# Kernel tuning notes

Hardware: AMD Instinct MI355X
Metric: run time of the kernel (lower is better)

The kernel has to match this reference:

```python
import jax, jax.numpy as jnp
import numpy as np

N, E = 50000, 800000
IN_CH, H, OUT_CH, ED, L = 64, 128, 128, 1, 4


def setup_inputs() -> dict:
    key = jax.random.key(0)
    ks = jax.random.split(key, 24)
    s = 0.02
    inp = {
        'h': jax.random.normal(ks[0], (N, IN_CH), jnp.float32),
        'coords': jax.random.normal(ks[1], (N, 3), jnp.float32),
        'edge_attr': jax.random.normal(ks[2], (E, ED), jnp.float32),
        'emb_in_W': jax.random.normal(ks[3], (IN_CH, H), jnp.float32) * s,
        'emb_in_b': jnp.zeros((H,), jnp.float32),
        'emb_out_W': jax.random.normal(ks[4], (H, OUT_CH), jnp.float32) * s,
        'emb_out_b': jnp.zeros((OUT_CH,), jnp.float32),
        # per-layer stacked params
        'eW1': jax.random.normal(ks[5], (L, 2 * H + 1 + ED, H), jnp.float32) * s,
        'eb1': jnp.zeros((L, H), jnp.float32),
        'eW2': jax.random.normal(ks[6], (L, H, H), jnp.float32) * s,
        'eb2': jnp.zeros((L, H), jnp.float32),
        'cW1': jax.random.normal(ks[7], (L, H, H), jnp.float32) * s,
        'cb1': jnp.zeros((L, H), jnp.float32),
        'cWc': jax.random.normal(ks[8], (L, H, 1), jnp.float32) * 0.001,  # xavier gain=0.001, no bias
        'nW1': jax.random.normal(ks[9], (L, 2 * H, H), jnp.float32) * s,
        'nb1': jnp.zeros((L, H), jnp.float32),
        'nW2': jax.random.normal(ks[10], (L, H, H), jnp.float32) * s,
        'nb2': jnp.zeros((L, H), jnp.float32),
        'edge_index': jax.random.randint(ks[11], (2, E), 0, N, jnp.int32),
    }
    return inp


def _egnn_forward(h, coords, edge_attr, emb_in_W, emb_in_b, emb_out_W, emb_out_b,
                  eW1, eb1, eW2, eb2, cW1, cb1, cWc, nW1, nb1, nW2, nb2, edge_index):
    silu = jax.nn.silu
    row, col = edge_index[0], edge_index[1]  # PyG: j=source=row, i=target=col
    # count of incoming edges per target node, for coords_agg='mean'
    counts = jax.ops.segment_sum(jnp.ones((E,), jnp.float32), col, num_segments=N)
    counts = jnp.maximum(counts, 1.0)[:, None]
    h = h @ emb_in_W + emb_in_b
    for l in range(L):
        coord_diff = coords[row] - coords[col]                       # [E,3]
        dist = jnp.sum(coord_diff * coord_diff, axis=-1, keepdims=True)  # [E,1]
        # message: edge MLP on cat(x_i, x_j, dist, edge_attr)
        edge_in = jnp.concatenate([h[col], h[row], dist, edge_attr], axis=-1)
        ef = silu(edge_in @ eW1[l] + eb1[l])
        ef = silu(ef @ eW2[l] + eb2[l])                               # [E,H]
        cw = silu(ef @ cW1[l] + cb1[l]) @ cWc[l]                      # [E,1]
        coord_upd = coord_diff * cw                                   # [E,3]
        # aggregate to target nodes
        agg_feat = jax.ops.segment_sum(ef, col, num_segments=N)       # [N,H]
        agg_coord = jax.ops.segment_sum(coord_upd, col, num_segments=N) / counts
        # node update (residual)
        node_in = jnp.concatenate([h, agg_feat], axis=-1)
        upd = silu(node_in @ nW1[l] + nb1[l]) @ nW2[l] + nb2[l]
        h = h + upd
        coords = coords + agg_coord
    h = h @ emb_out_W + emb_out_b
    return h, coords


def reference(h, coords, edge_attr, emb_in_W, emb_in_b, emb_out_W, emb_out_b,
              eW1, eb1, eW2, eb2, cW1, cb1, cWc, nW1, nb1, nW2, nb2, edge_index):
    return _egnn_forward(h, coords, edge_attr, emb_in_W, emb_in_b, emb_out_W, emb_out_b,
                         eW1, eb1, eW2, eb2, cW1, cb1, cWc, nW1, nb1, nW2, nb2, edge_index)
```

## Files before the change

### kernel.cpp

```cpp
#include <hip/hip_runtime.h>

constexpr int Nn = 50000;
constexpr int Ee = 800000;
constexpr int EF_STR  = 136;
constexpr int TL_STR  = 40;
constexpr int NIN_STR = 264;
constexpr int HIN_STR = 72;
constexpr int NB_SCAN = (Nn + 255) / 256;

typedef short s8v __attribute__((ext_vector_type(8)));
typedef float f4v __attribute__((ext_vector_type(4)));

__device__ __forceinline__ ushort f2bf(float f) {
    uint u = __float_as_uint(f);
    uint r = (u + 0x7FFFu + ((u >> 16) & 1u)) >> 16;
    return (ushort)r;
}
__device__ __forceinline__ ushort f2bf_t(float f) {
    return (ushort)(__float_as_uint(f) >> 16);
}
__device__ __forceinline__ float bf2f(ushort s) {
    return __uint_as_float(((uint)s) << 16);
}
__device__ __forceinline__ float silu_f(float x) {
    return x * __fdividef(1.0f, 1.0f + __expf(-x));
}
__device__ __forceinline__ uint pack2bf_t(float lo, float hi) {
    return __builtin_amdgcn_perm(__float_as_uint(hi), __float_as_uint(lo), 0x07060302u);
}
__device__ __forceinline__ uint pack2bf_r(float lo, float hi) {
    uint a = __float_as_uint(lo) + 0x8000u;
    uint b = __float_as_uint(hi) + 0x8000u;
    return __builtin_amdgcn_perm(b, a, 0x07060302u);
}

__device__ __forceinline__ void swz_one(const float* src, ushort* dst, int K, int KC, int idx)
{
    int per = KC * 4096;
    int l = idx / per, r = idx % per;
    int fb = r >> 9, rem = r & 511;
    int lane = rem >> 3, jj = rem & 7;
    int kc = fb >> 3, t = fb & 7;
    int k = kc * 32 + ((lane >> 4) << 3) + jj;
    int n = t * 16 + (lane & 15);
    float v = (k < K) ? src[(size_t)l * K * 128 + (size_t)k * 128 + n] : 0.0f;
    dst[idx] = f2bf(v);
}
__global__ void __launch_bounds__(256) k_swz_all(
    const float* __restrict__ eW1, const float* __restrict__ eW2, const float* __restrict__ cW1,
    const float* __restrict__ nW1, const float* __restrict__ nW2,
    const float* __restrict__ inW, const float* __restrict__ outW,
    ushort* __restrict__ o1, ushort* __restrict__ o2, ushort* __restrict__ o3,
    ushort* __restrict__ o4, ushort* __restrict__ o5,
    ushort* __restrict__ o6, ushort* __restrict__ o7)
{
    int gid = blockIdx.x * 256 + threadIdx.x;
    if (gid < 147456)      swz_one(eW1, o1, 258, 9, gid);
    else if (gid < 212992) swz_one(eW2, o2, 128, 4, gid - 147456);
    else if (gid < 278528) swz_one(cW1, o3, 128, 4, gid - 212992);
    else if (gid < 409600) swz_one(nW1, o4, 256, 8, gid - 278528);
    else if (gid < 475136) swz_one(nW2, o5, 128, 4, gid - 409600);
    else if (gid < 483328) swz_one(inW, o6, 64, 2, gid - 475136);
    else if (gid < 499712) swz_one(outW, o7, 128, 4, gid - 483328);
}

__global__ void __launch_bounds__(256) k_count(const int* __restrict__ eidx, int* __restrict__ ecnt)
{
    int e = blockIdx.x * 256 + threadIdx.x;
    atomicAdd(&ecnt[eidx[Ee + e]], 1);
}

__global__ void __launch_bounds__(256) k_bsum(const int* __restrict__ ecnt, int* __restrict__ bsum)
{
    __shared__ int ws[4];
    int tid = threadIdx.x, lane = tid & 63, w = tid >> 6;
    int i = blockIdx.x * 256 + tid;
    int x = (i < Nn) ? ecnt[i] : 0;
    #pragma unroll
    for (int off = 1; off < 64; off <<= 1) x += __shfl_xor(x, off, 64);
    if (lane == 0) ws[w] = x;
    __syncthreads();
    if (tid == 0) bsum[blockIdx.x] = ws[0] + ws[1] + ws[2] + ws[3];
}
__global__ void __launch_bounds__(256) k_bscan(int* __restrict__ bsum)
{
    __shared__ int ws[4];
    int tid = threadIdx.x, lane = tid & 63, w = tid >> 6;
    int x = (tid < NB_SCAN) ? bsum[tid] : 0;
    int s = x;
    #pragma unroll
    for (int off = 1; off < 64; off <<= 1) {
        int t = __shfl_up(s, off, 64);
        if (lane >= off) s += t;
    }
    if (lane == 63) ws[w] = s;
    __syncthreads();
    if (tid == 0) { int a = 0; for (int k = 0; k < 4; k++) { int t = ws[k]; ws[k] = a; a += t; } }
    __syncthreads();
    int excl = ws[w] + s - x;
    if (tid < NB_SCAN) bsum[tid] = excl;
}
__global__ void __launch_bounds__(256) k_cursor(const int* __restrict__ ecnt,
                                               const int* __restrict__ boff, int* __restrict__ cursor)
{
    __shared__ int ws[4];
    int tid = threadIdx.x, lane = tid & 63, w = tid >> 6;
    int i = blockIdx.x * 256 + tid;
    int x = (i < Nn) ? ecnt[i] : 0;
    int s = x;
    #pragma unroll
    for (int off = 1; off < 64; off <<= 1) {
        int t = __shfl_up(s, off, 64);
        if (lane >= off) s += t;
    }
    if (lane == 63) ws[w] = s;
    __syncthreads();
    if (tid == 0) { int a = 0; for (int k = 0; k < 4; k++) { int t = ws[k]; ws[k] = a; a += t; } }
    __syncthreads();
    int excl = ws[w] + s - x + boff[blockIdx.x];
    if (i < Nn) cursor[i] = excl;
}

__global__ void __launch_bounds__(256) k_scatter(
    const int* __restrict__ eidx, const float* __restrict__ edge_attr,
    int* __restrict__ cursor,
    int* __restrict__ srow, int* __restrict__ scol, float* __restrict__ sattr)
{
    int e = blockIdx.x * 256 + threadIdx.x;
    int r = eidx[e], c = eidx[Ee + e];
    int p = atomicAdd(&cursor[c], 1);
    srow[p] = r; scol[p] = c; sattr[p] = edge_attr[e];
}

__global__ void __launch_bounds__(512, 2) k_emb(
    const float* __restrict__ h_in, const float* __restrict__ coords,
    const ushort* __restrict__ ws_, const float* __restrict__ b,
    float* __restrict__ hbuf, ushort* __restrict__ hbf, float* __restrict__ cbuf)
{
    __shared__ alignas(16) ushort s_h[64 * HIN_STR];
    const int tid = threadIdx.x;
    const int nb = blockIdx.x * 64;
    #pragma unroll
    for (int i = 0; i < 2; i++) {
        int idx = i * 512 + tid;
        int e = idx >> 4, ch = idx & 15;
        int node = nb + e;
        float4 f = make_float4(0.f, 0.f, 0.f, 0.f);
        if (node < Nn) f = *(const float4*)(h_in + (size_t)node * 64 + ch * 4);
        ushort4 u; u.x = f2bf(f.x); u.y = f2bf(f.y); u.z = f2bf(f.z); u.w = f2bf(f.w);
        *(ushort4*)(s_h + e * HIN_STR + ch * 4) = u;
    }
    if (tid < 192) {
        int n = nb + tid / 3, d = tid % 3;
        if (n < Nn) cbuf[n * 3 + d] = coords[n * 3 + d];
    }
    __syncthreads();
    const int lane = tid & 63, wave = tid >> 6;
    const int m = lane & 15, quad = lane >> 4;
    const int ws2 = wave >> 2, wt = wave & 3;
    const int rbase = ws2 * 32;
    f4v acc[2][2];
    #pragma unroll
    for (int nt = 0; nt < 2; nt++) { acc[nt][0] = (f4v){0,0,0,0}; acc[nt][1] = (f4v){0,0,0,0}; }
    const ushort* aBase = ws_ + wt * 1024 + lane * 8;
    #pragma unroll
    for (int kc = 0; kc < 2; kc++) {
        s8v a0 = *(const s8v*)(aBase + kc * 4096);
        s8v a1 = *(const s8v*)(aBase + kc * 4096 + 512);
        #pragma unroll
        for (int nt = 0; nt < 2; nt++) {
            s8v bf = *(const s8v*)(s_h + (rbase + nt * 16 + m) * HIN_STR + kc * 32 + quad * 8);
            acc[nt][0] = __builtin_amdgcn_mfma_f32_16x16x32_bf16(a0, bf, acc[nt][0], 0, 0, 0);
            acc[nt][1] = __builtin_amdgcn_mfma_f32_16x16x32_bf16(a1, bf, acc[nt][1], 0, 0, 0);
        }
    }
    #pragma unroll
    for (int nt = 0; nt < 2; nt++) {
        int node = nb + rbase + nt * 16 + m;
        if (node < Nn) {
            #pragma unroll
            for (int ct = 0; ct < 2; ct++) {
                int colb = (wt * 2 + ct) * 16 + quad * 4;
                float4 bb = *(const float4*)(b + colb);
                float v0 = acc[nt][ct][0] + bb.x;
                float v1 = acc[nt][ct][1] + bb.y;
                float v2 = acc[nt][ct][2] + bb.z;
                float v3 = acc[nt][ct][3] + bb.w;
                *(float4*)(hbuf + (size_t)node * 128 + colb) = make_float4(v0, v1, v2, v3);
                uint2 pk; pk.x = pack2bf_r(v0, v1); pk.y = pack2bf_r(v2, v3);
                *(uint2*)(hbf + (size_t)node * 128 + colb) = pk;
            }
        }
    }
}

__global__ void __launch_bounds__(512, 8) k_edge(
    const ushort* __restrict__ hbf, const float* __restrict__ cbuf,
    const int* __restrict__ srow, const int* __restrict__ scol, const float* __restrict__ sattr,
    const ushort* __restrict__ w1s, const float* __restrict__ b1,
    const ushort* __restrict__ w2s, const float* __restrict__ b2,
    const ushort* __restrict__ cw1s, const float* __restrict__ cb1,
    const float* __restrict__ cwc,
    float* __restrict__ agg_feat, float* __restrict__ agg_coord)
{
    __shared__ alignas(16) ushort s_a[64 * EF_STR];
    __shared__ alignas(16) ushort s_b[64 * EF_STR];
    __shared__ alignas(16) ushort s_t[64 * TL_STR];
    __shared__ int   s_col[64];
    __shared__ float s_cd[64 * 3];

    const int tid = threadIdx.x;
    const int eb = blockIdx.x * 64;

    if (tid < 64) {
        int rw = srow[eb + tid], cl = scol[eb + tid];
        s_col[tid] = cl;
        float d0 = cbuf[rw * 3 + 0] - cbuf[cl * 3 + 0];
        float d1 = cbuf[rw * 3 + 1] - cbuf[cl * 3 + 1];
        float d2 = cbuf[rw * 3 + 2] - cbuf[cl * 3 + 2];
        s_cd[tid * 3 + 0] = d0; s_cd[tid * 3 + 1] = d1; s_cd[tid * 3 + 2] = d2;
        float dist = d0 * d0 + d1 * d1 + d2 * d2;
        s_t[tid * TL_STR + 0] = f2bf(dist);
        s_t[tid * TL_STR + 1] = f2bf(sattr[eb + tid]);
        uint* zp = (uint*)(s_t + tid * TL_STR + 2);
        #pragma unroll
        for (int z = 0; z < 15; z++) zp[z] = 0;
    }
    #pragma unroll
    for (int i = 0; i < 4; i++) {
        int idx = i * 512 + tid;
        int e = idx >> 5, ch = idx & 31;
        int node = (ch < 16) ? scol[eb + e] : srow[eb + e];
        uint4 v = *(const uint4*)(hbf + (size_t)node * 128 + (ch & 15) * 8);
        ushort* dst = (ch < 16) ? (s_a + e * EF_STR + ch * 8)
                                : (s_b + e * EF_STR + (ch - 16) * 8);
        *(uint4*)dst = v;
    }
    __syncthreads();

    const int lane = tid & 63, wave = tid >> 6;
    const int m = lane & 15, quad = lane >> 4;
    const int ws2 = wave >> 2, wt = wave & 3;
    const int rbase = ws2 * 32;

    f4v acc[2][2];
    {
        float bias0 = b1[wt * 32 + m], bias1 = b1[wt * 32 + 16 + m];
        #pragma unroll
        for (int mt = 0; mt < 2; mt++) {
            acc[mt][0] = (f4v){bias0, bias0, bias0, bias0};
            acc[mt][1] = (f4v){bias1, bias1, bias1, bias1};
        }
        const ushort* bBase = w1s + wt * 1024 + (size_t)lane * 8;
        #pragma unroll
        for (int kc = 0; kc < 4; kc++) {
            s8v b0 = *(const s8v*)(bBase + kc * 4096);
            s8v b1v = *(const s8v*)(bBase + kc * 4096 + 512);
            #pragma unroll
            for (int mt = 0; mt < 2; mt++) {
                s8v a = *(const s8v*)(s_a + (rbase + mt * 16 + m) * EF_STR + kc * 32 + quad * 8);
                acc[mt][0] = __builtin_amdgcn_mfma_f32_16x16x32_bf16(a, b0, acc[mt][0], 0, 0, 0);
                acc[mt][1] = __builtin_amdgcn_mfma_f32_16x16x32_bf16(a, b1v, acc[mt][1], 0, 0, 0);
            }
        }
        #pragma unroll
        for (int kc = 4; kc < 8; kc++) {
            s8v b0 = *(const s8v*)(bBase + kc * 4096);
            s8v b1v = *(const s8v*)(bBase + kc * 4096 + 512);
            #pragma unroll
            for (int mt = 0; mt < 2; mt++) {
                s8v a = *(const s8v*)(s_b + (rbase + mt * 16 + m) * EF_STR + (kc - 4) * 32 + quad * 8);
                acc[mt][0] = __builtin_amdgcn_mfma_f32_16x16x32_bf16(a, b0, acc[mt][0], 0, 0, 0);
                acc[mt][1] = __builtin_amdgcn_mfma_f32_16x16x32_bf16(a, b1v, acc[mt][1], 0, 0, 0);
            }
        }
        {
            s8v b0 = *(const s8v*)(bBase + 8 * 4096);
            s8v b1v = *(const s8v*)(bBase + 8 * 4096 + 512);
            #pragma unroll
            for (int mt = 0; mt < 2; mt++) {
                s8v a = *(const s8v*)(s_t + (rbase + mt * 16 + m) * TL_STR + quad * 8);
                acc[mt][0] = __builtin_amdgcn_mfma_f32_16x16x32_bf16(a, b0, acc[mt][0], 0, 0, 0);
                acc[mt][1] = __builtin_amdgcn_mfma_f32_16x16x32_bf16(a, b1v, acc[mt][1], 0, 0, 0);
            }
        }
    }
    __syncthreads();

    #pragma unroll
    for (int tt = 0; tt < 2; tt++) {
        int col = (wt * 2 + tt) * 16 + m;
        #pragma unroll
        for (int mt = 0; mt < 2; mt++)
            #pragma unroll
            for (int r = 0; r < 4; r++)
                s_a[(rbase + mt * 16 + quad * 4 + r) * EF_STR + col] = f2bf_t(silu_f(acc[mt][tt][r]));
    }
    __syncthreads();

    {
        f4v acc2[2][2];
        float bias0 = b2[wt * 32 + m], bias1 = b2[wt * 32 + 16 + m];
        #pragma unroll
        for (int mt = 0; mt < 2; mt++) {
            acc2[mt][0] = (f4v){bias0, bias0, bias0, bias0};
            acc2[mt][1] = (f4v){bias1, bias1, bias1, bias1};
        }
        const ushort* bBase = w2s + wt * 1024 + (size_t)lane * 8;
        #pragma unroll
        for (int kc = 0; kc < 4; kc++) {
            s8v b0 = *(const s8v*)(bBase + kc * 4096);
            s8v b1v = *(const s8v*)(bBase + kc * 4096 + 512);
            #pragma unroll
            for (int mt = 0; mt < 2; mt++) {
                s8v a = *(const s8v*)(s_a + (rbase + mt * 16 + m) * EF_STR + kc * 32 + quad * 8);
                acc2[mt][0] = __builtin_amdgcn_mfma_f32_16x16x32_bf16(a, b0, acc2[mt][0], 0, 0, 0);
                acc2[mt][1] = __builtin_amdgcn_mfma_f32_16x16x32_bf16(a, b1v, acc2[mt][1], 0, 0, 0);
            }
        }
        #pragma unroll
        for (int tt = 0; tt < 2; tt++) {
            int col = (wt * 2 + tt) * 16 + m;
            #pragma unroll
            for (int mt = 0; mt < 2; mt++)
                #pragma unroll
                for (int r = 0; r < 4; r++)
                    s_b[(rbase + mt * 16 + quad * 4 + r) * EF_STR + col] = f2bf_t(silu_f(acc2[mt][tt][r]));
        }
    }
    __syncthreads();

    {
        f4v acc3[2][2];
        float bias0 = cb1[wt * 32 + m], bias1 = cb1[wt * 32 + 16 + m];
        float wc0 = cwc[wt * 32 + m],  wc1 = cwc[wt * 32 + 16 + m];
        #pragma unroll
        for (int mt = 0; mt < 2; mt++) {
            acc3[mt][0] = (f4v){bias0, bias0, bias0, bias0};
            acc3[mt][1] = (f4v){bias1, bias1, bias1, bias1};
        }
        const ushort* bBase = cw1s + wt * 1024 + (size_t)lane * 8;
        #pragma unroll
        for (int kc = 0; kc < 4; kc++) {
            s8v b0 = *(const s8v*)(bBase + kc * 4096);
            s8v b1v = *(const s8v*)(bBase + kc * 4096 + 512);
            #pragma unroll
            for (int mt = 0; mt < 2; mt++) {
                s8v a = *(const s8v*)(s_b + (rbase + mt * 16 + m) * EF_STR + kc * 32 + quad * 8);
                acc3[mt][0] = __builtin_amdgcn_mfma_f32_16x16x32_bf16(a, b0, acc3[mt][0], 0, 0, 0);
                acc3[mt][1] = __builtin_amdgcn_mfma_f32_16x16x32_bf16(a, b1v, acc3[mt][1], 0, 0, 0);
            }
        }
        float* s_part = (float*)s_t;
        #pragma unroll
        for (int mt = 0; mt < 2; mt++)
            #pragma unroll
            for (int r = 0; r < 4; r++) {
                float p = silu_f(acc3[mt][0][r]) * wc0 + silu_f(acc3[mt][1][r]) * wc1;
                p += __shfl_xor(p, 1, 64);
                p += __shfl_xor(p, 2, 64);
                if ((m & 3) == 0) {
                    int slot = wt * 4 + (m >> 2);
                    s_part[(rbase + mt * 16 + quad * 4 + r) * 20 + slot] = p;
                }
            }
    }
    __syncthreads();

    if (tid < 64) {
        float* s_part = (float*)s_t;
        float cw = 0.0f;
        #pragma unroll
        for (int l = 0; l < 16; l++) cw += s_part[tid * 20 + l];
        int cn = s_col[tid];
        unsafeAtomicAdd(&agg_coord[cn * 3 + 0], s_cd[tid * 3 + 0] * cw);
        unsafeAtomicAdd(&agg_coord[cn * 3 + 1], s_cd[tid * 3 + 1] * cw);
        unsafeAtomicAdd(&agg_coord[cn * 3 + 2], s_cd[tid * 3 + 2] * cw);
    }
    if (tid < 256) {
        int j = tid & 127;
        int e0 = (tid >> 7) * 32;
        float accv = 0.0f; int cur = s_col[e0];
        #pragma unroll 4
        for (int e = e0; e < e0 + 32; e++) {
            int c = s_col[e];
            if (c != cur) {
                unsafeAtomicAdd(&agg_feat[(size_t)cur * 128 + j], accv);
                accv = 0.0f; cur = c;
            }
            accv += bf2f(s_b[e * EF_STR + j]);
        }
        unsafeAtomicAdd(&agg_feat[(size_t)cur * 128 + j], accv);
    }
}

__global__ void __launch_bounds__(512, 6) k_node(
    float* __restrict__ hbuf, ushort* __restrict__ hbf, float* __restrict__ cbuf,
    float* __restrict__ agg_feat, float* __restrict__ agg_coord,
    const int* __restrict__ ecnt,
    const ushort* __restrict__ w1s, const float* __restrict__ b1,
    const ushort* __restrict__ w2s, const float* __restrict__ b2)
{
    __shared__ alignas(16) ushort s_nin[64 * NIN_STR];
    __shared__ alignas(16) ushort s_t1[64 * EF_STR];
    const int tid = threadIdx.x;
    const int nb = blockIdx.x * 64;

    #pragma unroll
    for (int i = 0; i < 2; i++) {
        int idx = i * 512 + tid;
        int e = idx >> 4, ch = idx & 15;
        int node = nb + e;
        uint4 v = make_uint4(0, 0, 0, 0);
        if (node < Nn) v = *(const uint4*)(hbf + (size_t)node * 128 + ch * 8);
        *(uint4*)(s_nin + e * NIN_STR + ch * 8) = v;
    }
    #pragma unroll
    for (int i = 0; i < 4; i++) {
        int idx = i * 512 + tid;
        int e = idx >> 5, ch = idx & 31;
        int node = nb + e;
        float4 f = make_float4(0.f, 0.f, 0.f, 0.f);
        if (node < Nn) {
            f = *(const float4*)(agg_feat + (size_t)node * 128 + ch * 4);
            *(float4*)(agg_feat + (size_t)node * 128 + ch * 4) = make_float4(0.f, 0.f, 0.f, 0.f);
        }
        uint2 pk; pk.x = pack2bf_t(f.x, f.y); pk.y = pack2bf_t(f.z, f.w);
        *(uint2*)(s_nin + e * NIN_STR + 128 + ch * 4) = pk;
    }
    if (tid < 64) {
        int n = nb + tid;
        if (n < Nn) {
            float c = (float)ecnt[n]; c = (c < 1.0f) ? 1.0f : c;
            float inv = __fdividef(1.0f, c);
            cbuf[n * 3 + 0] += agg_coord[n * 3 + 0] * inv;
            cbuf[n * 3 + 1] += agg_coord[n * 3 + 1] * inv;
            cbuf[n * 3 + 2] += agg_coord[n * 3 + 2] * inv;
            agg_coord[n * 3 + 0] = 0.f; agg_coord[n * 3 + 1] = 0.f; agg_coord[n * 3 + 2] = 0.f;
        }
    }
    __syncthreads();

    const int lane = tid & 63, wave = tid >> 6;
    const int m = lane & 15, quad = lane >> 4;
    const int ws2 = wave >> 2, wt = wave & 3;
    const int rbase = ws2 * 32;

    {
        f4v acc[2][2];
        #pragma unroll
        for (int ct = 0; ct < 2; ct++) {
            float4 bb = *(const float4*)(b1 + (wt * 2 + ct) * 16 + quad * 4);
            acc[0][ct] = (f4v){bb.x, bb.y, bb.z, bb.w};
            acc[1][ct] = acc[0][ct];
        }
        const ushort* aBase = w1s + wt * 1024 + (size_t)lane * 8;
        #pragma unroll
        for (int kc = 0; kc < 8; kc++) {
            s8v a0 = *(const s8v*)(aBase + kc * 4096);
            s8v a1 = *(const s8v*)(aBase + kc * 4096 + 512);
            #pragma unroll
            for (int nt = 0; nt < 2; nt++) {
                s8v bf = *(const s8v*)(s_nin + (rbase + nt * 16 + m) * NIN_STR + kc * 32 + quad * 8);
                acc[nt][0] = __builtin_amdgcn_mfma_f32_16x16x32_bf16(a0, bf, acc[nt][0], 0, 0, 0);
                acc[nt][1] = __builtin_amdgcn_mfma_f32_16x16x32_bf16(a1, bf, acc[nt][1], 0, 0, 0);
            }
        }
        #pragma unroll
        for (int nt = 0; nt < 2; nt++) {
            int row = rbase + nt * 16 + m;
            #pragma unroll
            for (int ct = 0; ct < 2; ct++) {
                int colb = (wt * 2 + ct) * 16 + quad * 4;
                float v0 = silu_f(acc[nt][ct][0]);
                float v1 = silu_f(acc[nt][ct][1]);
                float v2 = silu_f(acc[nt][ct][2]);
                float v3 = silu_f(acc[nt][ct][3]);
                uint2 pk; pk.x = pack2bf_t(v0, v1); pk.y = pack2bf_t(v2, v3);
                *(uint2*)(s_t1 + row * EF_STR + colb) = pk;
            }
        }
    }
    __syncthreads();

    {
        f4v acc[2][2];
        #pragma unroll
        for (int ct = 0; ct < 2; ct++) {
            float4 bb = *(const float4*)(b2 + (wt * 2 + ct) * 16 + quad * 4);
            acc[0][ct] = (f4v){bb.x, bb.y, bb.z, bb.w};
            acc[1][ct] = acc[0][ct];
        }
        const ushort* aBase = w2s + wt * 1024 + (size_t)lane * 8;
        #pragma unroll
        for (int kc = 0; kc < 4; kc++) {
            s8v a0 = *(const s8v*)(aBase + kc * 4096);
            s8v a1 = *(const s8v*)(aBase + kc * 4096 + 512);
            #pragma unroll
            for (int nt = 0; nt < 2; nt++) {
                s8v bf = *(const s8v*)(s_t1 + (rbase + nt * 16 + m) * EF_STR + kc * 32 + quad * 8);
                acc[nt][0] = __builtin_amdgcn_mfma_f32_16x16x32_bf16(a0, bf, acc[nt][0], 0, 0, 0);
                acc[nt][1] = __builtin_amdgcn_mfma_f32_16x16x32_bf16(a1, bf, acc[nt][1], 0, 0, 0);
            }
        }
        #pragma unroll
        for (int nt = 0; nt < 2; nt++) {
            int node = nb + rbase + nt * 16 + m;
            if (node < Nn) {
                #pragma unroll
                for (int ct = 0; ct < 2; ct++) {
                    int colb = (wt * 2 + ct) * 16 + quad * 4;
                    float4 old = *(const float4*)(hbuf + (size_t)node * 128 + colb);
                    float v0 = old.x + acc[nt][ct][0];
                    float v1 = old.y + acc[nt][ct][1];
                    float v2 = old.z + acc[nt][ct][2];
                    float v3 = old.w + acc[nt][ct][3];
                    *(float4*)(hbuf + (size_t)node * 128 + colb) = make_float4(v0, v1, v2, v3);
                    uint2 pk; pk.x = pack2bf_r(v0, v1); pk.y = pack2bf_r(v2, v3);
                    *(uint2*)(hbf + (size_t)node * 128 + colb) = pk;
                }
            }
        }
    }
}

__global__ void __launch_bounds__(512, 2) k_emb_out(
    const ushort* __restrict__ hbf, const float* __restrict__ cbuf,
    const ushort* __restrict__ ws_, const float* __restrict__ b, float* __restrict__ out)
{
    __shared__ alignas(16) ushort s_h[64 * EF_STR];
    const int tid = threadIdx.x;
    const int nb = blockIdx.x * 64;
    #pragma unroll
    for (int i = 0; i < 2; i++) {
        int idx = i * 512 + tid;
        int e = idx >> 4, ch = idx & 15;
        int node = nb + e;
        uint4 v = make_uint4(0, 0, 0, 0);
        if (node < Nn) v = *(const uint4*)(hbf + (size_t)node * 128 + ch * 8);
        *(uint4*)(s_h + e * EF_STR + ch * 8) = v;
    }
    if (tid < 192) {
        int n = nb + tid / 3, d = tid % 3;
        if (n < Nn) out[(size_t)Nn * 128 + n * 3 + d] = cbuf[n * 3 + d];
    }
    __syncthreads();
    const int lane = tid & 63, wave = tid >> 6;
    const int m = lane & 15, quad = lane >> 4;
    const int ws2 = wave >> 2, wt = wave & 3;
    const int rbase = ws2 * 32;
    f4v acc[2][2];
    #pragma unroll
    for (int ct = 0; ct < 2; ct++) {
        float4 bb = *(const float4*)(b + (wt * 2 + ct) * 16 + quad * 4);
        acc[0][ct] = (f4v){bb.x, bb.y, bb.z, bb.w};
        acc[1][ct] = acc[0][ct];
    }
    const ushort* aBase = ws_ + wt * 1024 + (size_t)lane * 8;
    #pragma unroll
    for (int kc = 0; kc < 4; kc++) {
        s8v a0 = *(const s8v*)(aBase + kc * 4096);
        s8v a1 = *(const s8v*)(aBase + kc * 4096 + 512);
        #pragma unroll
        for (int nt = 0; nt < 2; nt++) {
            s8v bf = *(const s8v*)(s_h + (rbase + nt * 16 + m) * EF_STR + kc * 32 + quad * 8);
            acc[nt][0] = __builtin_amdgcn_mfma_f32_16x16x32_bf16(a0, bf, acc[nt][0], 0, 0, 0);
            acc[nt][1] = __builtin_amdgcn_mfma_f32_16x16x32_bf16(a1, bf, acc[nt][1], 0, 0, 0);
        }
    }
    #pragma unroll
    for (int nt = 0; nt < 2; nt++) {
        int node = nb + rbase + nt * 16 + m;
        if (node < Nn) {
            #pragma unroll
            for (int ct = 0; ct < 2; ct++) {
                int colb = (wt * 2 + ct) * 16 + quad * 4;
                float4 o = make_float4(acc[nt][ct][0], acc[nt][ct][1],
                                       acc[nt][ct][2], acc[nt][ct][3]);
                *(float4*)(out + (size_t)node * 128 + colb) = o;
            }
        }
    }
}

extern "C" void kernel_launch(void* const* d_in, const int* in_sizes, int n_in,
                              void* d_out, int out_size, void* d_ws, size_t ws_size,
                              hipStream_t stream)
{
    const float* h_in      = (const float*)d_in[0];
    const float* coords    = (const float*)d_in[1];
    const float* edge_attr = (const float*)d_in[2];
    const float* emb_in_W  = (const float*)d_in[3];
    const float* emb_in_b  = (const float*)d_in[4];
    const float* emb_out_W = (const float*)d_in[5];
    const float* emb_out_b = (const float*)d_in[6];
    const float* eW1 = (const float*)d_in[7];
    const float* eb1 = (const float*)d_in[8];
    const float* eW2 = (const float*)d_in[9];
    const float* eb2 = (const float*)d_in[10];
    const float* cW1 = (const float*)d_in[11];
    const float* cb1 = (const float*)d_in[12];
    const float* cWc = (const float*)d_in[13];
    const float* nW1 = (const float*)d_in[14];
    const float* nb1 = (const float*)d_in[15];
    const float* nW2 = (const float*)d_in[16];
    const float* nb2 = (const float*)d_in[17];
    const int*  eidx = (const int*)d_in[18];

    size_t off = 0;
    char* base = (char*)d_ws;
    auto alloc = [&](size_t bytes) -> char* {
        char* p = base + off;
        off += (bytes + 255) & ~(size_t)255;
        return p;
    };
    float*  hbuf      = (float*)alloc((size_t)Nn * 128 * 4);
    ushort* hbf       = (ushort*)alloc((size_t)Nn * 128 * 2);
    float*  cbuf      = (float*)alloc((size_t)Nn * 3 * 4);
    int*    ecnt      = (int*)alloc((size_t)Nn * 4);
    int*    cursor    = (int*)alloc((size_t)Nn * 4);
    int*    bsum      = (int*)alloc((size_t)NB_SCAN * 4);
    int*    srow      = (int*)alloc((size_t)Ee * 4);
    int*    scol      = (int*)alloc((size_t)Ee * 4);
    float*  sattr     = (float*)alloc((size_t)Ee * 4);
    float*  agg_feat  = (float*)alloc((size_t)Nn * 128 * 4);
    float*  agg_coord = (float*)alloc((size_t)Nn * 3 * 4);
    ushort* eW1s      = (ushort*)alloc((size_t)4 * 36864 * 2);
    ushort* eW2s      = (ushort*)alloc((size_t)4 * 16384 * 2);
    ushort* cW1s      = (ushort*)alloc((size_t)4 * 16384 * 2);
    ushort* nW1s      = (ushort*)alloc((size_t)4 * 32768 * 2);
    ushort* nW2s      = (ushort*)alloc((size_t)4 * 16384 * 2);
    ushort* eInWs     = (ushort*)alloc((size_t)8192 * 2);
    ushort* eOutWs    = (ushort*)alloc((size_t)16384 * 2);

    k_swz_all<<<499712 / 256, 256, 0, stream>>>(
        eW1, eW2, cW1, nW1, nW2, emb_in_W, emb_out_W,
        eW1s, eW2s, cW1s, nW1s, nW2s, eInWs, eOutWs);

    hipMemsetAsync(ecnt, 0, (size_t)Nn * 4, stream);
    k_count<<<Ee / 256, 256, 0, stream>>>(eidx, ecnt);
    k_bsum<<<NB_SCAN, 256, 0, stream>>>(ecnt, bsum);
    k_bscan<<<1, 256, 0, stream>>>(bsum);
    k_cursor<<<NB_SCAN, 256, 0, stream>>>(ecnt, bsum, cursor);
    k_scatter<<<Ee / 256, 256, 0, stream>>>(eidx, edge_attr, cursor, srow, scol, sattr);
    k_emb<<<(Nn + 63) / 64, 512, 0, stream>>>(h_in, coords, eInWs, emb_in_b, hbuf, hbf, cbuf);

    hipMemsetAsync(agg_feat, 0, (size_t)Nn * 128 * 4, stream);
    hipMemsetAsync(agg_coord, 0, (size_t)Nn * 3 * 4, stream);

    for (int l = 0; l < 4; l++) {
        k_edge<<<Ee / 64, 512, 0, stream>>>(
            hbf, cbuf, srow, scol, sattr,
            eW1s + (size_t)l * 36864, eb1 + l * 128,
            eW2s + (size_t)l * 16384, eb2 + l * 128,
            cW1s + (size_t)l * 16384, cb1 + l * 128,
            cWc + l * 128,
            agg_feat, agg_coord);
        k_node<<<(Nn + 63) / 64, 512, 0, stream>>>(
            hbuf, hbf, cbuf, agg_feat, agg_coord, ecnt,
            nW1s + (size_t)l * 32768, nb1 + l * 128,
            nW2s + (size_t)l * 16384, nb2 + l * 128);
    }
    k_emb_out<<<(Nn + 63) / 64, 512, 0, stream>>>(hbf, cbuf, eOutWs, emb_out_b, (float*)d_out);
}
```

Measured before the change: 1.676 ms.

## Factor first edge-MLP layer into per-node projections gathered per edge

```diff
diff --git a/kernel.cpp b/kernel.cpp
--- a/kernel.cpp
+++ b/kernel.cpp
@@ -3,7 +3,6 @@
 constexpr int Nn = 50000;
 constexpr int Ee = 800000;
 constexpr int EF_STR  = 136;
-constexpr int TL_STR  = 40;
 constexpr int NIN_STR = 264;
 constexpr int HIN_STR = 72;
 constexpr int NB_SCAN = (Nn + 255) / 256;
@@ -34,7 +33,7 @@
     return __builtin_amdgcn_perm(b, a, 0x07060302u);
 }
 
-__device__ __forceinline__ void swz_one(const float* src, ushort* dst, int K, int KC, int idx)
+__device__ __forceinline__ void swz_one(const float* src, ushort* dst, int K, int lstride, int KC, int idx)
 {
     int per = KC * 4096;
     int l = idx / per, r = idx % per;
@@ -43,25 +42,27 @@
     int kc = fb >> 3, t = fb & 7;
     int k = kc * 32 + ((lane >> 4) << 3) + jj;
     int n = t * 16 + (lane & 15);
-    float v = (k < K) ? src[(size_t)l * K * 128 + (size_t)k * 128 + n] : 0.0f;
+    float v = (k < K) ? src[(size_t)l * lstride + (size_t)k * 128 + n] : 0.0f;
     dst[idx] = f2bf(v);
 }
 __global__ void __launch_bounds__(256) k_swz_all(
     const float* __restrict__ eW1, const float* __restrict__ eW2, const float* __restrict__ cW1,
     const float* __restrict__ nW1, const float* __restrict__ nW2,
     const float* __restrict__ inW, const float* __restrict__ outW,
-    ushort* __restrict__ o1, ushort* __restrict__ o2, ushort* __restrict__ o3,
+    ushort* __restrict__ oT, ushort* __restrict__ oM,
+    ushort* __restrict__ o2, ushort* __restrict__ o3,
     ushort* __restrict__ o4, ushort* __restrict__ o5,
     ushort* __restrict__ o6, ushort* __restrict__ o7)
 {
     int gid = blockIdx.x * 256 + threadIdx.x;
-    if (gid < 147456)      swz_one(eW1, o1, 258, 9, gid);
-    else if (gid < 212992) swz_one(eW2, o2, 128, 4, gid - 147456);
-    else if (gid < 278528) swz_one(cW1, o3, 128, 4, gid - 212992);
-    else if (gid < 409600) swz_one(nW1, o4, 256, 8, gid - 278528);
-    else if (gid < 475136) swz_one(nW2, o5, 128, 4, gid - 409600);
-    else if (gid < 483328) swz_one(inW, o6, 64, 2, gid - 475136);
-    else if (gid < 499712) swz_one(outW, o7, 128, 4, gid - 483328);
+    if (gid < 65536)       swz_one(eW1,         oT, 128, 33024, 4, gid);
+    else if (gid < 131072) swz_one(eW1 + 16384, oM, 128, 33024, 4, gid - 65536);
+    else if (gid < 196608) swz_one(eW2, o2, 128, 16384, 4, gid - 131072);
+    else if (gid < 262144) swz_one(cW1, o3, 128, 16384, 4, gid - 196608);
+    else if (gid < 393216) swz_one(nW1, o4, 256, 32768, 8, gid - 262144);
+    else if (gid < 458752) swz_one(nW2, o5, 128, 16384, 4, gid - 393216);
+    else if (gid < 466944) swz_one(inW, o6, 64, 8192, 2, gid - 458752);
+    else if (gid < 483328) swz_one(outW, o7, 128, 16384, 4, gid - 466944);
 }
 
 __global__ void __launch_bounds__(256) k_count(const int* __restrict__ eidx, int* __restrict__ ecnt)
@@ -194,10 +195,77 @@
     }
 }
 
+__global__ void __launch_bounds__(512, 2) k_uv(
+    const ushort* __restrict__ hbf,
+    const ushort* __restrict__ topW, const ushort* __restrict__ midW,
+    const float* __restrict__ b1, ushort* __restrict__ uvb)
+{
+    __shared__ alignas(16) ushort s_h[64 * EF_STR];
+    const int tid = threadIdx.x;
+    const int nb = blockIdx.x * 64;
+    #pragma unroll
+    for (int i = 0; i < 2; i++) {
+        int idx = i * 512 + tid;
+        int e = idx >> 4, ch = idx & 15;
+        int node = nb + e;
+        uint4 v = make_uint4(0, 0, 0, 0);
+        if (node < Nn) v = *(const uint4*)(hbf + (size_t)node * 128 + ch * 8);
+        *(uint4*)(s_h + e * EF_STR + ch * 8) = v;
+    }
+    __syncthreads();
+    const int lane = tid & 63, wave = tid >> 6;
+    const int m = lane & 15, quad = lane >> 4;
+    const int ws2 = wave >> 2, wt = wave & 3;
+    const int rbase = ws2 * 32;
+    f4v au[2][2], av[2][2];
+    #pragma unroll
+    for (int ct = 0; ct < 2; ct++) {
+        float4 bb = *(const float4*)(b1 + (wt * 2 + ct) * 16 + quad * 4);
+        au[0][ct] = (f4v){bb.x, bb.y, bb.z, bb.w};
+        au[1][ct] = au[0][ct];
+        av[0][ct] = (f4v){0,0,0,0};
+        av[1][ct] = (f4v){0,0,0,0};
+    }
+    const ushort* tBase = topW + wt * 1024 + (size_t)lane * 8;
+    const ushort* mBase = midW + wt * 1024 + (size_t)lane * 8;
+    #pragma unroll
+    for (int kc = 0; kc < 4; kc++) {
+        s8v t0 = *(const s8v*)(tBase + kc * 4096);
+        s8v t1 = *(const s8v*)(tBase + kc * 4096 + 512);
+        s8v m0 = *(const s8v*)(mBase + kc * 4096);
+        s8v m1 = *(const s8v*)(mBase + kc * 4096 + 512);
+        #pragma unroll
+        for (int nt = 0; nt < 2; nt++) {
+            s8v bf = *(const s8v*)(s_h + (rbase + nt * 16 + m) * EF_STR + kc * 32 + quad * 8);
+            au[nt][0] = __builtin_amdgcn_mfma_f32_16x16x32_bf16(t0, bf, au[nt][0], 0, 0, 0);
+            au[nt][1] = __builtin_amdgcn_mfma_f32_16x16x32_bf16(t1, bf, au[nt][1], 0, 0, 0);
+            av[nt][0] = __builtin_amdgcn_mfma_f32_16x16x32_bf16(m0, bf, av[nt][0], 0, 0, 0);
+            av[nt][1] = __builtin_amdgcn_mfma_f32_16x16x32_bf16(m1, bf, av[nt][1], 0, 0, 0);
+        }
+    }
+    #pragma unroll
+    for (int nt = 0; nt < 2; nt++) {
+        int node = nb + rbase + nt * 16 + m;
+        if (node < Nn) {
+            #pragma unroll
+            for (int ct = 0; ct < 2; ct++) {
+                int colb = (wt * 2 + ct) * 16 + quad * 4;
+                uint2 pu; pu.x = pack2bf_r(au[nt][ct][0], au[nt][ct][1]);
+                          pu.y = pack2bf_r(au[nt][ct][2], au[nt][ct][3]);
+                *(uint2*)(uvb + (size_t)node * 256 + colb) = pu;
+                uint2 pv; pv.x = pack2bf_r(av[nt][ct][0], av[nt][ct][1]);
+                          pv.y = pack2bf_r(av[nt][ct][2], av[nt][ct][3]);
+                *(uint2*)(uvb + (size_t)node * 256 + 128 + colb) = pv;
+            }
+        }
+    }
+}
+
 __global__ void __launch_bounds__(512, 8) k_edge(
-    const ushort* __restrict__ hbf, const float* __restrict__ cbuf,
+    const float* __restrict__ cbuf,
     const int* __restrict__ srow, const int* __restrict__ scol, const float* __restrict__ sattr,
-    const ushort* __restrict__ w1s, const float* __restrict__ b1,
+    const ushort* __restrict__ uvb,
+    const float* __restrict__ wd, const float* __restrict__ wa,
     const ushort* __restrict__ w2s, const float* __restrict__ b2,
     const ushort* __restrict__ cw1s, const float* __restrict__ cb1,
     const float* __restrict__ cwc,
@@ -205,7 +273,7 @@
 {
     __shared__ alignas(16) ushort s_a[64 * EF_STR];
     __shared__ alignas(16) ushort s_b[64 * EF_STR];
-    __shared__ alignas(16) ushort s_t[64 * TL_STR];
+    __shared__ alignas(16) float  s_t[64 * 20];
     __shared__ int   s_col[64];
     __shared__ float s_cd[64 * 3];
 
@@ -219,22 +287,47 @@
         float d1 = cbuf[rw * 3 + 1] - cbuf[cl * 3 + 1];
         float d2 = cbuf[rw * 3 + 2] - cbuf[cl * 3 + 2];
         s_cd[tid * 3 + 0] = d0; s_cd[tid * 3 + 1] = d1; s_cd[tid * 3 + 2] = d2;
-        float dist = d0 * d0 + d1 * d1 + d2 * d2;
-        s_t[tid * TL_STR + 0] = f2bf(dist);
-        s_t[tid * TL_STR + 1] = f2bf(sattr[eb + tid]);
-        uint* zp = (uint*)(s_t + tid * TL_STR + 2);
-        #pragma unroll
-        for (int z = 0; z < 15; z++) zp[z] = 0;
-    }
-    #pragma unroll
-    for (int i = 0; i < 4; i++) {
-        int idx = i * 512 + tid;
-        int e = idx >> 5, ch = idx & 31;
-        int node = (ch < 16) ? scol[eb + e] : srow[eb + e];
-        uint4 v = *(const uint4*)(hbf + (size_t)node * 128 + (ch & 15) * 8);
-        ushort* dst = (ch < 16) ? (s_a + e * EF_STR + ch * 8)
-                                : (s_b + e * EF_STR + (ch - 16) * 8);
-        *(uint4*)dst = v;
+        s_t[tid * 20 + 16] = d0 * d0 + d1 * d1 + d2 * d2;
+        s_t[tid * 20 + 17] = sattr[eb + tid];
+        s_t[tid * 20 + 18] = __int_as_float(rw);
+    }
+    __syncthreads();
+
+    {
+        const int e = tid >> 3, ch = tid & 7;
+        float dist = s_t[e * 20 + 16];
+        float attr = s_t[e * 20 + 17];
+        int row = __float_as_int(s_t[e * 20 + 18]);
+        int col = s_col[e];
+        const ushort* up = uvb + (size_t)col * 256 + ch * 16;
+        const ushort* vp = uvb + (size_t)row * 256 + 128 + ch * 16;
+        uint4 ua = *(const uint4*)up;
+        uint4 ub = *(const uint4*)(up + 8);
+        uint4 va = *(const uint4*)vp;
+        uint4 vb = *(const uint4*)(vp + 8);
+        float4 wdv[4], wav[4];
+        #pragma unroll
+        for (int i = 0; i < 4; i++) {
+            wdv[i] = *(const float4*)(wd + ch * 16 + i * 4);
+            wav[i] = *(const float4*)(wa + ch * 16 + i * 4);
+        }
+        const float* wdf = (const float*)wdv;
+        const float* waf = (const float*)wav;
+        uint uu[8] = {ua.x, ua.y, ua.z, ua.w, ub.x, ub.y, ub.z, ub.w};
+        uint vv[8] = {va.x, va.y, va.z, va.w, vb.x, vb.y, vb.z, vb.w};
+        uint pk[8];
+        #pragma unroll
+        for (int p = 0; p < 8; p++) {
+            float ulo = __uint_as_float(uu[p] << 16);
+            float uhi = __uint_as_float(uu[p] & 0xFFFF0000u);
+            float vlo = __uint_as_float(vv[p] << 16);
+            float vhi = __uint_as_float(vv[p] & 0xFFFF0000u);
+            float lo = ulo + vlo + dist * wdf[2 * p] + attr * waf[2 * p];
+            float hi = uhi + vhi + dist * wdf[2 * p + 1] + attr * waf[2 * p + 1];
+            pk[p] = pack2bf_t(silu_f(lo), silu_f(hi));
+        }
+        *(uint4*)(s_a + e * EF_STR + ch * 16) = make_uint4(pk[0], pk[1], pk[2], pk[3]);
+        *(uint4*)(s_a + e * EF_STR + ch * 16 + 8) = make_uint4(pk[4], pk[5], pk[6], pk[7]);
     }
     __syncthreads();
 
@@ -243,61 +336,6 @@
     const int ws2 = wave >> 2, wt = wave & 3;
     const int rbase = ws2 * 32;
 
-    f4v acc[2][2];
-    {
-        float bias0 = b1[wt * 32 + m], bias1 = b1[wt * 32 + 16 + m];
-        #pragma unroll
-        for (int mt = 0; mt < 2; mt++) {
-            acc[mt][0] = (f4v){bias0, bias0, bias0, bias0};
-            acc[mt][1] = (f4v){bias1, bias1, bias1, bias1};
-        }
-        const ushort* bBase = w1s + wt * 1024 + (size_t)lane * 8;
-        #pragma unroll
-        for (int kc = 0; kc < 4; kc++) {
-            s8v b0 = *(const s8v*)(bBase + kc * 4096);
-            s8v b1v = *(const s8v*)(bBase + kc * 4096 + 512);
-            #pragma unroll
-            for (int mt = 0; mt < 2; mt++) {
-                s8v a = *(const s8v*)(s_a + (rbase + mt * 16 + m) * EF_STR + kc * 32 + quad * 8);
-                acc[mt][0] = __builtin_amdgcn_mfma_f32_16x16x32_bf16(a, b0, acc[mt][0], 0, 0, 0);
-                acc[mt][1] = __builtin_amdgcn_mfma_f32_16x16x32_bf16(a, b1v, acc[mt][1], 0, 0, 0);
-            }
-        }
-        #pragma unroll
-        for (int kc = 4; kc < 8; kc++) {
-            s8v b0 = *(const s8v*)(bBase + kc * 4096);
-            s8v b1v = *(const s8v*)(bBase + kc * 4096 + 512);
-            #pragma unroll
-            for (int mt = 0; mt < 2; mt++) {
-                s8v a = *(const s8v*)(s_b + (rbase + mt * 16 + m) * EF_STR + (kc - 4) * 32 + quad * 8);
-                acc[mt][0] = __builtin_amdgcn_mfma_f32_16x16x32_bf16(a, b0, acc[mt][0], 0, 0, 0);
-                acc[mt][1] = __builtin_amdgcn_mfma_f32_16x16x32_bf16(a, b1v, acc[mt][1], 0, 0, 0);
-            }
-        }
-        {
-            s8v b0 = *(const s8v*)(bBase + 8 * 4096);
-            s8v b1v = *(const s8v*)(bBase + 8 * 4096 + 512);
-            #pragma unroll
-            for (int mt = 0; mt < 2; mt++) {
-                s8v a = *(const s8v*)(s_t + (rbase + mt * 16 + m) * TL_STR + quad * 8);
-                acc[mt][0] = __builtin_amdgcn_mfma_f32_16x16x32_bf16(a, b0, acc[mt][0], 0, 0, 0);
-                acc[mt][1] = __builtin_amdgcn_mfma_f32_16x16x32_bf16(a, b1v, acc[mt][1], 0, 0, 0);
-            }
-        }
-    }
-    __syncthreads();
-
-    #pragma unroll
-    for (int tt = 0; tt < 2; tt++) {
-        int col = (wt * 2 + tt) * 16 + m;
-        #pragma unroll
-        for (int mt = 0; mt < 2; mt++)
-            #pragma unroll
-            for (int r = 0; r < 4; r++)
-                s_a[(rbase + mt * 16 + quad * 4 + r) * EF_STR + col] = f2bf_t(silu_f(acc[mt][tt][r]));
-    }
-    __syncthreads();
-
     {
         f4v acc2[2][2];
         float bias0 = b2[wt * 32 + m], bias1 = b2[wt * 32 + 16 + m];
@@ -351,7 +389,6 @@
                 acc3[mt][1] = __builtin_amdgcn_mfma_f32_16x16x32_bf16(a, b1v, acc3[mt][1], 0, 0, 0);
             }
         }
-        float* s_part = (float*)s_t;
         #pragma unroll
         for (int mt = 0; mt < 2; mt++)
             #pragma unroll
@@ -361,17 +398,16 @@
                 p += __shfl_xor(p, 2, 64);
                 if ((m & 3) == 0) {
                     int slot = wt * 4 + (m >> 2);
-                    s_part[(rbase + mt * 16 + quad * 4 + r) * 20 + slot] = p;
+                    s_t[(rbase + mt * 16 + quad * 4 + r) * 20 + slot] = p;
                 }
             }
     }
     __syncthreads();
 
     if (tid < 64) {
-        float* s_part = (float*)s_t;
         float cw = 0.0f;
         #pragma unroll
-        for (int l = 0; l < 16; l++) cw += s_part[tid * 20 + l];
+        for (int l = 0; l < 16; l++) cw += s_t[tid * 20 + l];
         int cn = s_col[tid];
         unsafeAtomicAdd(&agg_coord[cn * 3 + 0], s_cd[tid * 3 + 0] * cw);
         unsafeAtomicAdd(&agg_coord[cn * 3 + 1], s_cd[tid * 3 + 1] * cw);
@@ -616,6 +652,7 @@
     };
     float*  hbuf      = (float*)alloc((size_t)Nn * 128 * 4);
     ushort* hbf       = (ushort*)alloc((size_t)Nn * 128 * 2);
+    ushort* uvb       = (ushort*)alloc((size_t)Nn * 256 * 2);
     float*  cbuf      = (float*)alloc((size_t)Nn * 3 * 4);
     int*    ecnt      = (int*)alloc((size_t)Nn * 4);
     int*    cursor    = (int*)alloc((size_t)Nn * 4);
@@ -625,7 +662,8 @@
     float*  sattr     = (float*)alloc((size_t)Ee * 4);
     float*  agg_feat  = (float*)alloc((size_t)Nn * 128 * 4);
     float*  agg_coord = (float*)alloc((size_t)Nn * 3 * 4);
-    ushort* eW1s      = (ushort*)alloc((size_t)4 * 36864 * 2);
+    ushort* eW1tops   = (ushort*)alloc((size_t)4 * 16384 * 2);
+    ushort* eW1mids   = (ushort*)alloc((size_t)4 * 16384 * 2);
     ushort* eW2s      = (ushort*)alloc((size_t)4 * 16384 * 2);
     ushort* cW1s      = (ushort*)alloc((size_t)4 * 16384 * 2);
     ushort* nW1s      = (ushort*)alloc((size_t)4 * 32768 * 2);
@@ -633,9 +671,9 @@
     ushort* eInWs     = (ushort*)alloc((size_t)8192 * 2);
     ushort* eOutWs    = (ushort*)alloc((size_t)16384 * 2);
 
-    k_swz_all<<<499712 / 256, 256, 0, stream>>>(
+    k_swz_all<<<483328 / 256, 256, 0, stream>>>(
         eW1, eW2, cW1, nW1, nW2, emb_in_W, emb_out_W,
-        eW1s, eW2s, cW1s, nW1s, nW2s, eInWs, eOutWs);
+        eW1tops, eW1mids, eW2s, cW1s, nW1s, nW2s, eInWs, eOutWs);
 
     hipMemsetAsync(ecnt, 0, (size_t)Nn * 4, stream);
     k_count<<<Ee / 256, 256, 0, stream>>>(eidx, ecnt);
@@ -649,9 +687,13 @@
     hipMemsetAsync(agg_coord, 0, (size_t)Nn * 3 * 4, stream);
 
     for (int l = 0; l < 4; l++) {
+        k_uv<<<(Nn + 63) / 64, 512, 0, stream>>>(
+            hbf, eW1tops + (size_t)l * 16384, eW1mids + (size_t)l * 16384,
+            eb1 + l * 128, uvb);
         k_edge<<<Ee / 64, 512, 0, stream>>>(
-            hbf, cbuf, srow, scol, sattr,
-            eW1s + (size_t)l * 36864, eb1 + l * 128,
+            cbuf, srow, scol, sattr, uvb,
+            eW1 + ((size_t)l * 258 + 256) * 128,
+            eW1 + ((size_t)l * 258 + 257) * 128,
             eW2s + (size_t)l * 16384, eb2 + l * 128,
             cW1s + (size_t)l * 16384, cb1 + l * 128,
             cWc + l * 128,
```

Result: no change. 1.647 ms (-1.8%).
